# Kernel tuning notes

Hardware: AMD Instinct MI355X
Metric: run time of the kernel (lower is better)

## Reference

```python
import jax, jax.numpy as jnp
import numpy as np
from jax.scipy.special import gammaln, digamma


def setup_inputs() -> dict:
    key = jax.random.key(0)
    k1, k2 = jax.random.split(key)
    N, M, D = 512, 512, 256
    # Dirichlet concentration parameters: strictly positive
    v_alpha = jax.random.uniform(k1, (N, D), dtype=jnp.float32)
    t_alpha = jax.random.uniform(k2, (M, D), dtype=jnp.float32)
    return {"v_alpha": v_alpha, "t_alpha": t_alpha}


def _compute_kl(v_alpha, t_alpha):
    # v_alpha, t_alpha broadcast to (..., D); returns (...,) KL(Dir(v)||Dir(t))
    eps = 1e-08
    v = v_alpha + eps
    t = t_alpha + eps
    sum_v = v.sum(axis=-1)
    sum_t = t.sum(axis=-1)
    first = (gammaln(t).sum(axis=-1) + gammaln(sum_v)
             - gammaln(sum_t) - gammaln(v).sum(axis=-1))
    second = ((v - t) * (digamma(v) - digamma(sum_v)[..., None])).sum(axis=-1)
    return first + second


def reference(v_alpha, t_alpha):
    # Pairwise JS divergence between all (t_row, v_row) pairs.
    # Original: v.repeat(M,1) / t.repeat_interleave(N) then view(M, N)
    # -> equivalent to broadcasting t over axis 0, v over axis 1.
    v = v_alpha[None, :, :]   # (1, N, D)
    t = t_alpha[:, None, :]   # (M, 1, D)
    m = 0.5 * (v + t)         # (M, N, D)
    jsd = 0.5 * _compute_kl(v, m) + 0.5 * _compute_kl(t, m)  # (M, N)
    return 1.0 - jsd
```

## Files before the change

### kernel.cpp

```cpp
#include <hip/hip_runtime.h>

#define D 256
#define NV 512
#define NT 512
#define KCAT 1536
#define EPS 1e-8f
#define HALF_EPS 5e-9f
#define LN2 0.69314718055994531f

#define C0 0.28468287047291920f
#define C1 0.70315664064524320f
#define C2 0.24517887805011740f
#define C3 (-0.03936734194028790f)
#define C4 0.00932941036738560f
#define C5 (-0.00261463332905590f)
#define C6 0.00080356830356760f
#define C0E 0.28460998445f
#define C1E 0.69577526404f
#define C2E 0.24751123064f

#define LSTRIDE 68

typedef float f32x4 __attribute__((ext_vector_type(4)));
typedef short s16x8 __attribute__((ext_vector_type(8)));
typedef unsigned short u16;

__device__ __forceinline__ float rcpf(float x) { return __builtin_amdgcn_rcpf(x); }

__device__ __forceinline__ u16 f2bf(float f) {
    unsigned int u = __float_as_uint(f);
    return (u16)((u + 0x7FFFu + ((u >> 16) & 1u)) >> 16);
}
__device__ __forceinline__ float bf2f(u16 b) {
    return __uint_as_float(((unsigned int)b) << 16);
}

__device__ __forceinline__ float stirling_lgamma(float y) {
    float r = rcpf(y), r2 = r * r;
    float ln = LN2 * __log2f(y);
    return (y - 0.5f) * ln - y + 0.91893853320467f
         + r * (0.08333333333f - 0.00277777778f * r2);
}

__device__ __forceinline__ float stirling_digamma(float y) {
    float r = rcpf(y), r2 = r * r;
    return LN2 * __log2f(y) - 0.5f * r - r2 * (0.08333333333f - 0.00833333333f * r2);
}

__device__ __forceinline__ int tidx(int s, int d, int rr) {
    return (((s << 5) + (d >> 3)) * 512 + rr) * 8 + (d & 7);
}

__global__ __launch_bounds__(256) void row_stats(
    const float* __restrict__ va, const float* __restrict__ ta,
    u16* __restrict__ AcatT, u16* __restrict__ BcatT,
    float* __restrict__ rv, float* __restrict__ rt)
{
    int r = blockIdx.x;
    bool isV = (r < NV);
    int rr = isV ? r : r - NV;
    const float* row = (isV ? va : ta) + rr * D;
    float* sc = (isV ? rv : rt) + rr * 4;
    u16* cat = isV ? BcatT : AcatT;

    int d = threadIdx.x;
    float raw = row[d];
    float x = raw + EPS;

    float y = x + 4.0f;
    float ry = rcpf(y), ry2 = ry * ry;
    float psi = LN2 * __log2f(y) - 0.5f * ry - ry2 * (0.08333333333f - 0.00833333333f * ry2);
    psi -= rcpf(x) + rcpf(x + 1.0f) + rcpf(x + 2.0f) + rcpf(x + 3.0f);

    float s = x - 0.5f;
    float q6 = fmaf(C6, s, C5);
    q6 = fmaf(q6, s, C4); q6 = fmaf(q6, s, C3); q6 = fmaf(q6, s, C2); q6 = fmaf(q6, s, C1);
    float g = fmaf(q6, s, C0) - LN2 * __log2f(x * (x + 1.0f));

    float pm = psi - C2E * x;
    u16 xh = f2bf(x);  u16 xl = f2bf(x - bf2f(xh));
    u16 ph = f2bf(pm); u16 pl = f2bf(pm - bf2f(ph));
    if (isV) {
        cat[tidx(0,d,rr)] = ph; cat[tidx(1,d,rr)] = pl; cat[tidx(2,d,rr)] = ph;
        cat[tidx(3,d,rr)] = xh; cat[tidx(4,d,rr)] = xl; cat[tidx(5,d,rr)] = xh;
    } else {
        cat[tidx(0,d,rr)] = xh; cat[tidx(1,d,rr)] = xh; cat[tidx(2,d,rr)] = xl;
        cat[tidx(3,d,rr)] = ph; cat[tidx(4,d,rr)] = ph; cat[tidx(5,d,rr)] = pl;
    }

    float vh = fmaf(0.5f, raw, HALF_EPS);
    float S = raw, G = g, P = x * psi, Q = vh * vh;
    #pragma unroll
    for (int off = 32; off > 0; off >>= 1) {
        S += __shfl_down(S, off, 64);
        G += __shfl_down(G, off, 64);
        P += __shfl_down(P, off, 64);
        Q += __shfl_down(Q, off, 64);
    }
    __shared__ float red[4][4];
    int wid = d >> 6, lane = d & 63;
    if (lane == 0) { red[0][wid] = S; red[1][wid] = G; red[2][wid] = P; red[3][wid] = Q; }
    __syncthreads();
    if (d == 0) {
        float S4 = red[0][0] + red[0][1] + red[0][2] + red[0][3];
        float G4 = red[1][0] + red[1][1] + red[1][2] + red[1][3];
        float P4 = red[2][0] + red[2][1] + red[2][2] + red[2][3];
        float Q4 = red[3][0] + red[3][1] + red[3][2] + red[3][3];
        float Se = S4 + 256.0f * EPS;
        float A = 0.5f * (stirling_lgamma(Se) - G4) + 0.25f * P4;
        *(float4*)sc = make_float4(S4, A, stirling_digamma(Se), Q4);
    }
}

__global__ __launch_bounds__(256, 4) void jsd_pairs(
    const float* __restrict__ va, const float* __restrict__ ta,
    const u16* __restrict__ AcatT, const u16* __restrict__ BcatT,
    const float* __restrict__ rv, const float* __restrict__ rt,
    float* __restrict__ out)
{
    __shared__ float vs[16 * LSTRIDE];
    __shared__ float ts[16 * LSTRIDE];
    __shared__ float red[4 * 256];

    const int tid = threadIdx.x;
    const int j0 = blockIdx.x * 16;
    const int i0 = blockIdx.y * 16;
    const int w = tid >> 6, l = tid & 63;

    const int tj = tid & 15;
    const int ti = tid >> 4;

    float4 cv = *(const float4*)(va + (j0 + ti) * D + (tj << 2));
    float4 ct = *(const float4*)(ta + (i0 + ti) * D + (tj << 2));

    {
        f32x4 acc = {0.0f, 0.0f, 0.0f, 0.0f};
        const u16* Ap = AcatT + (((w * 48 + (l >> 4)) * 512) + i0 + (l & 15)) * 8;
        const u16* Bp = BcatT + (((w * 48 + (l >> 4)) * 512) + j0 + (l & 15)) * 8;
        #pragma unroll
        for (int st = 0; st < 12; ++st) {
            s16x8 a = *(const s16x8*)(Ap + st * 16384);
            s16x8 b = *(const s16x8*)(Bp + st * 16384);
            acc = __builtin_amdgcn_mfma_f32_16x16x32_bf16(a, b, acc, 0, 0, 0);
        }
        int base = w * 256 + ((l >> 4) << 6) + (l & 15);
        red[base]      = acc[0];
        red[base + 16] = acc[1];
        red[base + 32] = acc[2];
        red[base + 48] = acc[3];
    }

    const float* vp = vs + tj * LSTRIDE;
    const float* tp = ts + ti * LSTRIDE;
    const int ldst = ti * LSTRIDE + (tj << 2);

    float acc0 = 0.0f, acc1 = 0.0f, acc2 = 0.0f, acc3 = 0.0f;

    #define HALVE4(P) { P.x = fmaf(0.5f,P.x,HALF_EPS); P.y = fmaf(0.5f,P.y,HALF_EPS); \
                        P.z = fmaf(0.5f,P.z,HALF_EPS); P.w = fmaf(0.5f,P.w,HALF_EPS); }

    #define CITER(c, ACC) {                                                   \
        float4 v4 = *(const float4*)(vp + ((c) << 2));                        \
        float4 t4 = *(const float4*)(tp + ((c) << 2));                        \
        float m0 = v4.x + t4.x, m1 = v4.y + t4.y;                             \
        float m2 = v4.z + t4.z, m3 = v4.w + t4.w;                             \
        float w0 = fmaf(m0, m0, m0), w1 = fmaf(m1, m1, m1);                   \
        float w2 = fmaf(m2, m2, m2), w3 = fmaf(m3, m3, m3);                   \
        ACC += __log2f((w0 * w1) * (w2 * w3)); }

    #pragma unroll 1
    for (int h = 0; h < 4; ++h) {
        if (h) __syncthreads();
        float4 sv = cv, st4 = ct;
        HALVE4(sv); HALVE4(st4);
        *(float4*)(vs + ldst) = sv;
        *(float4*)(ts + ldst) = st4;
        if (h < 3) {
            int goff = ((h + 1) << 6) + (tj << 2);
            cv = *(const float4*)(va + (j0 + ti) * D + goff);
            ct = *(const float4*)(ta + (i0 + ti) * D + goff);
        }
        __syncthreads();
        CITER(0, acc0)  CITER(1, acc1)  CITER(2, acc2)  CITER(3, acc3)
        CITER(4, acc0)  CITER(5, acc1)  CITER(6, acc2)  CITER(7, acc3)
        CITER(8, acc0)  CITER(9, acc1)  CITER(10, acc2) CITER(11, acc3)
        CITER(12, acc0) CITER(13, acc1) CITER(14, acc2) CITER(15, acc3)
    }

    const int idx = ti * 16 + tj;
    float W = red[idx] + red[256 + idx] + red[512 + idx] + red[768 + idx];

    const int j = j0 + tj, i = i0 + ti;
    float4 RJ = *(const float4*)(rv + j * 4);
    float4 RI = *(const float4*)(rt + i * 4);
    float Sv = RJ.x, Av = RJ.y, dgSv = RJ.z, Qv = RJ.w;
    float St = RI.x, At = RI.y, dgSt = RI.z, Qt = RI.w;

    float M1 = fmaf(0.5f, Sv + St, 256.0f * EPS);
    float S1 = M1 - 128.0f;
    float quad = Qv + Qt - M1 + 64.0f;
    float sumlg = fmaf(C1E, S1, 256.0f * C0E) + C2E * quad
                - LN2 * ((acc0 + acc1) + (acc2 + acc3));

    float jsd = sumlg - stirling_lgamma(M1) + Av + At
              - 0.25f * W
              + 0.25f * (Sv - St) * (dgSt - dgSv);

    out[i * 512 + j] = 1.0f - jsd;
}

extern "C" void kernel_launch(void* const* d_in, const int* in_sizes, int n_in,
                              void* d_out, int out_size, void* d_ws, size_t ws_size,
                              hipStream_t stream) {
    const float* va = (const float*)d_in[0];
    const float* ta = (const float*)d_in[1];
    float* ws  = (float*)d_ws;
    float* rv  = ws;
    float* rt  = ws + NV * 4;
    u16*   AcatT = (u16*)((char*)d_ws + 16384);
    u16*   BcatT = (u16*)((char*)d_ws + 16384 + NV * KCAT * 2);
    float* out = (float*)d_out;

    row_stats<<<NV + NT, 256, 0, stream>>>(va, ta, AcatT, BcatT, rv, rt);
    jsd_pairs<<<dim3(32, 32), 256, 0, stream>>>(va, ta, AcatT, BcatT, rv, rt, out);
}
```

Measured before the change: 71.44 us.

## Split the D reduction across two blocks and combine partial results with atomics

Adds a z-dimension of 2 to the pair grid so each block handles half of the feature dimension and half of the MFMA K-slices. Partial sums are combined with atomicAdd into an output zeroed by a memset, and only the h==0 block adds the per-row terms. The occupancy hint is raised from 4 to 8 blocks per CU. The aim is more parallelism from the 1024-block grid. The cost is an extra memset, global atomics and a less deterministic floating-point sum order.

New measurement: 71.67 us. No clear change (+0.3%).

```diff
diff --git a/kernel.cpp b/kernel.cpp
--- a/kernel.cpp
+++ b/kernel.cpp
@@ -112,7 +112,7 @@
     }
 }
 
-__global__ __launch_bounds__(256, 4) void jsd_pairs(
+__global__ __launch_bounds__(256, 8) void jsd_pairs(
     const float* __restrict__ va, const float* __restrict__ ta,
     const u16* __restrict__ AcatT, const u16* __restrict__ BcatT,
     const float* __restrict__ rv, const float* __restrict__ rt,
@@ -125,20 +125,24 @@
     const int tid = threadIdx.x;
     const int j0 = blockIdx.x * 16;
     const int i0 = blockIdx.y * 16;
+    const int h  = blockIdx.z;
     const int w = tid >> 6, l = tid & 63;
 
     const int tj = tid & 15;
     const int ti = tid >> 4;
 
-    float4 cv = *(const float4*)(va + (j0 + ti) * D + (tj << 2));
-    float4 ct = *(const float4*)(ta + (i0 + ti) * D + (tj << 2));
+    const float* vbase = va + (j0 + ti) * D + h * 128;
+    const float* tbase = ta + (i0 + ti) * D + h * 128;
+    float4 cv = *(const float4*)(vbase + (tj << 2));
+    float4 ct = *(const float4*)(tbase + (tj << 2));
 
     {
         f32x4 acc = {0.0f, 0.0f, 0.0f, 0.0f};
-        const u16* Ap = AcatT + (((w * 48 + (l >> 4)) * 512) + i0 + (l & 15)) * 8;
-        const u16* Bp = BcatT + (((w * 48 + (l >> 4)) * 512) + j0 + (l & 15)) * 8;
+        const int cbase = h * 96 + w * 24 + (l >> 4);
+        const u16* Ap = AcatT + ((cbase * 512) + i0 + (l & 15)) * 8;
+        const u16* Bp = BcatT + ((cbase * 512) + j0 + (l & 15)) * 8;
         #pragma unroll
-        for (int st = 0; st < 12; ++st) {
+        for (int st = 0; st < 6; ++st) {
             s16x8 a = *(const s16x8*)(Ap + st * 16384);
             s16x8 b = *(const s16x8*)(Bp + st * 16384);
             acc = __builtin_amdgcn_mfma_f32_16x16x32_bf16(a, b, acc, 0, 0, 0);
@@ -169,16 +173,15 @@
         ACC += __log2f((w0 * w1) * (w2 * w3)); }
 
     #pragma unroll 1
-    for (int h = 0; h < 4; ++h) {
-        if (h) __syncthreads();
+    for (int p = 0; p < 2; ++p) {
+        if (p) __syncthreads();
         float4 sv = cv, st4 = ct;
         HALVE4(sv); HALVE4(st4);
         *(float4*)(vs + ldst) = sv;
         *(float4*)(ts + ldst) = st4;
-        if (h < 3) {
-            int goff = ((h + 1) << 6) + (tj << 2);
-            cv = *(const float4*)(va + (j0 + ti) * D + goff);
-            ct = *(const float4*)(ta + (i0 + ti) * D + goff);
+        if (p == 0) {
+            cv = *(const float4*)(vbase + 64 + (tj << 2));
+            ct = *(const float4*)(tbase + 64 + (tj << 2));
         }
         __syncthreads();
         CITER(0, acc0)  CITER(1, acc1)  CITER(2, acc2)  CITER(3, acc3)
@@ -189,24 +192,25 @@
 
     const int idx = ti * 16 + tj;
     float W = red[idx] + red[256 + idx] + red[512 + idx] + red[768 + idx];
+    float accL = (acc0 + acc1) + (acc2 + acc3);
 
     const int j = j0 + tj, i = i0 + ti;
-    float4 RJ = *(const float4*)(rv + j * 4);
-    float4 RI = *(const float4*)(rt + i * 4);
-    float Sv = RJ.x, Av = RJ.y, dgSv = RJ.z, Qv = RJ.w;
-    float St = RI.x, At = RI.y, dgSt = RI.z, Qt = RI.w;
-
-    float M1 = fmaf(0.5f, Sv + St, 256.0f * EPS);
-    float S1 = M1 - 128.0f;
-    float quad = Qv + Qt - M1 + 64.0f;
-    float sumlg = fmaf(C1E, S1, 256.0f * C0E) + C2E * quad
-                - LN2 * ((acc0 + acc1) + (acc2 + acc3));
-
-    float jsd = sumlg - stirling_lgamma(M1) + Av + At
-              - 0.25f * W
-              + 0.25f * (Sv - St) * (dgSt - dgSv);
-
-    out[i * 512 + j] = 1.0f - jsd;
+
+    float val = LN2 * accL + 0.25f * W;
+    if (h == 0) {
+        float4 RJ = *(const float4*)(rv + j * 4);
+        float4 RI = *(const float4*)(rt + i * 4);
+        float Sv = RJ.x, Av = RJ.y, dgSv = RJ.z, Qv = RJ.w;
+        float St = RI.x, At = RI.y, dgSt = RI.z, Qt = RI.w;
+        float M1 = fmaf(0.5f, Sv + St, 256.0f * EPS);
+        float S1 = M1 - 128.0f;
+        float quad = Qv + Qt - M1 + 64.0f;
+        float SC = fmaf(C1E, S1, 256.0f * C0E) + C2E * quad
+                 - stirling_lgamma(M1) + Av + At
+                 + 0.25f * (Sv - St) * (dgSt - dgSv);
+        val += 1.0f - SC;
+    }
+    atomicAdd(&out[i * 512 + j], val);
 }
 
 extern "C" void kernel_launch(void* const* d_in, const int* in_sizes, int n_in,
@@ -221,6 +225,7 @@
     u16*   BcatT = (u16*)((char*)d_ws + 16384 + NV * KCAT * 2);
     float* out = (float*)d_out;
 
+    hipMemsetAsync(out, 0, 512 * 512 * sizeof(float), stream);
     row_stats<<<NV + NT, 256, 0, stream>>>(va, ta, AcatT, BcatT, rv, rt);
-    jsd_pairs<<<dim3(32, 32), 256, 0, stream>>>(va, ta, AcatT, BcatT, rv, rt, out);
-}
+    jsd_pairs<<<dim3(32, 32, 2), 256, 0, stream>>>(va, ta, AcatT, BcatT, rv, rt, out);
+}
```
